# Kernel tuning notes

Measured on AMD Instinct MI355X. Metric: run time of the kernel, lower is better.

Reference implementation:

```python
import jax, jax.numpy as jnp
import numpy as np

E, S, D, A, L, H, C = 8, 6000, 128, 16, 64, 256, 64
B = 50            # no_batches hardcoded in torch forward
T = S // B        # number of outer integration steps
DT = 0.5          # solver dt; t_horizon=[0,1] -> 2 reversible-Heun substeps
NSUB = 2
SQDT = float(np.sqrt(DT))


def setup_inputs():
    ks = jax.random.split(jax.random.key(0), 24)
    w = lambda k, shp, s=0.05: (jax.random.normal(k, shp) * s).astype(jnp.float32)
    z = lambda shp: jnp.zeros(shp, jnp.float32)
    return dict(
        xs=w(ks[0], (E, S, D), 1.0),
        actions=w(ks[1], (E, S, A), 1.0),
        z0_noise=w(ks[2], (T, E, B, L), 1.0),
        dW=w(ks[3], (T, NSUB, E * B, L), 1.0),
        enc_w1=w(ks[4], (E, D, H)), enc_b1=z((E, H)),
        enc_w2=w(ks[5], (E, H, C)), enc_b2=z((E, C)),
        qz0_w=w(ks[6], (E, C, 2 * L)), qz0_b=z((E, 2 * L)),
        act_w=w(ks[7], (E, L + A + D, L)), act_b=z((E, L)),
        fw1=w(ks[8], (L, H)), fb1=z((H,)),
        fw2=w(ks[9], (H, H)), fb2=z((H,)),
        fw3=w(ks[10], (H, L)), fb3=z((L,)),
        hw1=w(ks[11], (L, H)), hb1=z((H,)),
        hw2=w(ks[12], (H, H)), hb2=z((H,)),
        hw3=w(ks[13], (H, L)), hb3=z((L,)),
        gw1=w(ks[14], (L, H)), gb1=z((L, H)),
        gw2=w(ks[15], (L, H), 0.02), gb2=jnp.ones((L,), jnp.float32),
        pw1=w(ks[16], (E, L, H)), pb1=z((E, H)),
        pw2=w(ks[17], (E, H, H)), pb2=z((E, H)),
        pw3=w(ks[18], (E, H, D)), pb3=z((E, D)),
        pz0_mean=z((E, 1, L)), pz0_logstd=z((E, 1, L)),
    )


def reference(xs, actions, z0_noise, dW,
              enc_w1, enc_b1, enc_w2, enc_b2, qz0_w, qz0_b, act_w, act_b,
              fw1, fb1, fw2, fb2, fw3, fb3, hw1, hb1, hw2, hb2, hw3, hb3,
              gw1, gb1, gw2, gb2, pw1, pb1, pw2, pb2, pw3, pb3,
              pz0_mean, pz0_logstd):
    xs_r = xs.reshape(E, T, B, D).transpose(1, 0, 2, 3)       # [T,E,B,D]
    act_r = actions.reshape(E, T, B, A).transpose(1, 0, 2, 3)  # [T,E,B,A]

    def mlp3(y, w1, b1, w2, b2, w3, b3):
        h1 = jax.nn.sigmoid(y @ w1 + b1)
        h2 = jax.nn.sigmoid(h1 @ w2 + b2)
        return h2 @ w3 + b3

    def g_fn(y):  # per-latent-dim diagonal diffusion nets, vectorized over L
        hc = jax.nn.sigmoid(y[..., None] * gw1 + gb1)          # [N,L,H]
        return jnp.sum(hc * gw2, axis=-1) + gb2                # [N,L]

    def drift_all(zc):
        fz = mlp3(zc, fw1, fb1, fw2, fb2, fw3, fb3)
        hz = mlp3(zc, hw1, hb1, hw2, hb2, hw3, hb3)
        gz = g_fn(zc)
        u = (fz - hz) / gz
        return fz, gz, 0.5 * jnp.sum(u * u, axis=-1)           # logqp drift

    def sde_solve(zini, dWs):  # reversible Heun, Stratonovich, logqp-augmented
        zc = zh = zini
        lc = lh = jnp.zeros(zini.shape[0], zini.dtype)
        fz, gz, lf = drift_all(zc)
        for k in range(NSUB):
            dWk = dWs[k] * SQDT
            zh_n = 2.0 * zc - zh + fz * DT + gz * dWk
            lh_n = 2.0 * lc - lh + lf * DT
            fz1, gz1, lf1 = drift_all(zh_n)
            zc = zc + 0.5 * (fz + fz1) * DT + 0.5 * (gz + gz1) * dWk
            lc = lc + 0.5 * (lf + lf1) * DT
            zh, lh, fz, gz, lf = zh_n, lh_n, fz1, gz1, lf1
        return zc, lc

    def step(z_prev, inp):
        i, x_i, a_i, n_i, dW_i = inp
        c1 = jax.nn.sigmoid(jnp.einsum('ebd,edh->ebh', x_i, enc_w1) + enc_b1[:, None])
        ctx = jnp.einsum('ebh,ehc->ebc', c1, enc_w2) + enc_b2[:, None]
        q = jnp.einsum('ebc,eck->ebk', ctx, qz0_w) + qz0_b[:, None]
        qm, ql = q[..., :L], q[..., L:]
        z0 = qm + jnp.exp(ql) * n_i
        z_in = jnp.where(i == 0, z0, z_prev)
        lat = jnp.concatenate([z_in, a_i, x_i], axis=-1)
        z_enc = jnp.einsum('ebf,efl->ebl', lat, act_w) + act_b[:, None]
        zf, lr = sde_solve(z_enc.reshape(E * B, L), dW_i)
        z_new = zf.reshape(E, B, L)
        p1 = jax.nn.sigmoid(jnp.einsum('ebl,elh->ebh', z_new, pw1) + pb1[:, None])
        p2 = jax.nn.sigmoid(jnp.einsum('ebh,ehk->ebk', p1, pw2) + pb2[:, None])
        xm = jnp.einsum('ebh,ehd->ebd', p2, pw3) + pb3[:, None]
        # KL(q(z0) || p(z0)) elementwise, p has mean pz0_mean, logstd pz0_logstd
        kl = (pz0_logstd - ql
              + (jnp.exp(2.0 * ql) + (qm - pz0_mean) ** 2) / (2.0 * jnp.exp(2.0 * pz0_logstd))
              - 0.5)
        logqp0 = kl.sum(-1).mean(-1)  # [E]
        return z_new, (xm, lr.reshape(E, B), logqp0)

    z_init = jnp.zeros((E, B, L), xs.dtype)
    _, (xm_all, lr_all, lq0_all) = jax.lax.scan(
        step, z_init, (jnp.arange(T), xs_r, act_r, z0_noise, dW))
    predicted_xs = xm_all.transpose(1, 0, 2, 3).reshape(E, T * B, D)
    logqp_path = lr_all.mean(-1).sum(0) + lq0_all.sum(0)  # [E]
    return logqp_path, predicted_xs
```

## Files before the change

### kernel.cpp

```cpp
#include <hip/hip_runtime.h>
#include <math.h>

#define E 8
#define S 6000
#define D 128
#define A 16
#define L 64
#define H 256
#define C 64
#define B 50
#define T 120
#define NSUB 2
#define FLAT 208
#define RTOT 400
#define RPB 10
#define NBLK (RTOT / RPB)
#define BGRP 10
#define NBG 5

#define DT 0.5f
#define SQDT 0.70710678118654752440f

#define GNT 4096
#define GYMIN (-128.0f)
#define GDY 0.0625f
#define GINVDY 16.0f

typedef __attribute__((ext_vector_type(8))) short bf16x8;
typedef __attribute__((ext_vector_type(4))) float f32x4;

#define MFMA16(a, b, c) __builtin_amdgcn_mfma_f32_16x16x32_bf16(a, b, c, 0, 0, 0)

__device__ __forceinline__ float sigf(float x) { return 1.0f / (1.0f + __expf(-x)); }

__device__ __forceinline__ unsigned short f2bf(float x) {
    union { float f; unsigned u; } v; v.f = x;
    unsigned r = (v.u + 0x7FFFu + ((v.u >> 16) & 1u)) >> 16;
    return (unsigned short)r;
}

__device__ __forceinline__ void bar_lgkm() {
    asm volatile("s_waitcnt lgkmcnt(0)" ::: "memory");
    __builtin_amdgcn_s_barrier();
    __builtin_amdgcn_sched_barrier(0);
}

__global__ void gtab_kernel(const float* __restrict__ gw1, const float* __restrict__ gb1,
                            const float* __restrict__ gw2, const float* __restrict__ gb2,
                            float* __restrict__ tab) {
    int idx = blockIdx.x * blockDim.x + threadIdx.x;
    if (idx >= L * GNT) return;
    int l = idx / GNT, i = idx % GNT;
    float y = GYMIN + (float)i * GDY;
    const float* w1 = gw1 + l * H;
    const float* b1 = gb1 + l * H;
    const float* w2 = gw2 + l * H;
    float acc = gb2[l];
    #pragma unroll 4
    for (int h = 0; h < H; ++h) acc += w2[h] * sigf(y * w1[h] + b1[h]);
    tab[idx] = acc;
}

__global__ void packB_kernel(const float* __restrict__ src, unsigned short* __restrict__ dst,
                             int K, int N) {
    int idx = blockIdx.x * 256 + threadIdx.x;
    if (idx >= K * N) return;
    int j = idx & 7;
    int lane = (idx >> 3) & 63;
    int t2 = idx >> 9;
    int KC = K >> 5;
    int kc = t2 % KC, n = t2 / KC;
    int k = (kc << 5) + ((lane >> 4) << 3) + j;
    int c = (n << 4) + (lane & 15);
    dst[idx] = f2bf(src[k * N + c]);
}

__global__ void packAW_kernel(const float* __restrict__ aw, unsigned short* __restrict__ dst) {
    int idx = blockIdx.x * 256 + threadIdx.x;
    if (idx >= E * L * L) return;
    int e = idx >> 12;
    int rem = idx & 4095;
    int j = rem & 7;
    int lane = (rem >> 3) & 63;
    int t2 = rem >> 9;
    int kc = t2 & 1, n = t2 >> 1;
    int k = (kc << 5) + ((lane >> 4) << 3) + j;
    int c = (n << 4) + (lane & 15);
    dst[idx] = f2bf(aw[((size_t)e * FLAT + k) * L + c]);
}

__global__ __launch_bounds__(256) void enc_kernel(const float* __restrict__ xs, const float* __restrict__ z0n,
                           const float* __restrict__ ew1, const float* __restrict__ eb1,
                           const float* __restrict__ ew2, const float* __restrict__ eb2,
                           const float* __restrict__ qw,  const float* __restrict__ qb,
                           const float* __restrict__ pm,  const float* __restrict__ pl,
                           float* __restrict__ z0buf, float* __restrict__ logqp0p) {
    int bid = blockIdx.x;
    int bg = bid % NBG; int te = bid / NBG; int e = te % E; int t = te / E;
    int tid = threadIdx.x;
    __shared__ float xsh[BGRP][D];
    __shared__ float c1s[BGRP][H];
    __shared__ float part[4][C][BGRP];
    __shared__ float ctxs[BGRP][C];
    __shared__ float qs[BGRP][2 * L];

    for (int i = tid; i < BGRP * D; i += 256) {
        int j = i / D, d = i % D;
        xsh[j][d] = xs[((size_t)e * S + (size_t)t * B + bg * BGRP + j) * D + d];
    }
    __syncthreads();
    {
        float bias = eb1[e * H + tid];
        float acc[BGRP];
        #pragma unroll
        for (int j = 0; j < BGRP; ++j) acc[j] = bias;
        const float* w = ew1 + (size_t)e * D * H + tid;
        #pragma unroll 4
        for (int d = 0; d < D; ++d) {
            float wv = w[(size_t)d * H];
            #pragma unroll
            for (int j = 0; j < BGRP; ++j) acc[j] += xsh[j][d] * wv;
        }
        #pragma unroll
        for (int j = 0; j < BGRP; ++j) c1s[j][tid] = sigf(acc[j]);
    }
    __syncthreads();
    {
        int c = tid & 63, kq = tid >> 6;
        float acc[BGRP];
        #pragma unroll
        for (int j = 0; j < BGRP; ++j) acc[j] = 0.f;
        const float* w = ew2 + (size_t)e * H * C + c;
        #pragma unroll 4
        for (int h = kq * 64; h < kq * 64 + 64; ++h) {
            float wv = w[(size_t)h * C];
            #pragma unroll
            for (int j = 0; j < BGRP; ++j) acc[j] += c1s[j][h] * wv;
        }
        #pragma unroll
        for (int j = 0; j < BGRP; ++j) part[kq][c][j] = acc[j];
    }
    __syncthreads();
    if (tid < C) {
        float bias = eb2[e * C + tid];
        #pragma unroll
        for (int j = 0; j < BGRP; ++j)
            ctxs[j][tid] = part[0][tid][j] + part[1][tid][j] + part[2][tid][j] + part[3][tid][j] + bias;
    }
    __syncthreads();
    if (tid < 2 * L) {
        float bias = qb[e * 2 * L + tid];
        float acc[BGRP];
        #pragma unroll
        for (int j = 0; j < BGRP; ++j) acc[j] = bias;
        const float* w = qw + (size_t)e * C * 2 * L + tid;
        #pragma unroll 4
        for (int c = 0; c < C; ++c) {
            float wv = w[(size_t)c * 2 * L];
            #pragma unroll
            for (int j = 0; j < BGRP; ++j) acc[j] += ctxs[j][c] * wv;
        }
        #pragma unroll
        for (int j = 0; j < BGRP; ++j) qs[j][tid] = acc[j];
    }
    __syncthreads();
    if (tid < L) {
        int l = tid;
        float kacc = 0.f;
        float m = pm[e * L + l], ls = pl[e * L + l];
        float inv2e = 1.0f / (2.0f * __expf(2.0f * ls));
        #pragma unroll
        for (int j = 0; j < BGRP; ++j) {
            float qm = qs[j][l], ql = qs[j][L + l];
            if (t == 0) {
                int b = bg * BGRP + j;
                float n = z0n[((size_t)e * B + b) * L + l];
                z0buf[((size_t)e * B + b) * L + l] = qm + __expf(ql) * n;
            }
            float dq = qm - m;
            kacc += ls - ql + (__expf(2.f * ql) + dq * dq) * inv2e - 0.5f;
        }
        #pragma unroll
        for (int off = 32; off; off >>= 1) kacc += __shfl_xor(kacc, off);
        if (l == 0) logqp0p[bid] = kacc / (float)B;
    }
}

__global__ __launch_bounds__(64) void ax_kernel(const float* __restrict__ xs, const float* __restrict__ actions,
                          const float* __restrict__ aw, const float* __restrict__ ab,
                          float* __restrict__ ax) {
    int bid = blockIdx.x;
    int bg = bid % NBG; int te = bid / NBG; int e = te % E; int t = te / E;
    int tid = threadIdx.x;
    __shared__ float xrow[BGRP][D];
    __shared__ float arow[BGRP][A];
    for (int i = tid; i < BGRP * D; i += 64) {
        int j = i / D, d = i % D;
        xrow[j][d] = xs[((size_t)e * S + (size_t)t * B + bg * BGRP + j) * D + d];
    }
    for (int i = tid; i < BGRP * A; i += 64) {
        int j = i / A, a = i % A;
        arow[j][a] = actions[((size_t)e * S + (size_t)t * B + bg * BGRP + j) * A + a];
    }
    __syncthreads();
    int l = tid;
    float acc[BGRP];
    float bias = ab[e * L + l];
    #pragma unroll
    for (int j = 0; j < BGRP; ++j) acc[j] = bias;
    const float* awp = aw + ((size_t)e * FLAT + L) * L + l;
    #pragma unroll 4
    for (int a = 0; a < A; ++a) {
        float wv = awp[(size_t)a * L];
        #pragma unroll
        for (int j = 0; j < BGRP; ++j) acc[j] += arow[j][a] * wv;
    }
    const float* xwp = aw + ((size_t)e * FLAT + L + A) * L + l;
    #pragma unroll 4
    for (int d = 0; d < D; ++d) {
        float wv = xwp[(size_t)d * L];
        #pragma unroll
        for (int j = 0; j < BGRP; ++j) acc[j] += xrow[j][d] * wv;
    }
    size_t rbase = (size_t)t * RTOT + e * B + bg * BGRP;
    #pragma unroll
    for (int j = 0; j < BGRP; ++j) ax[(rbase + j) * L + l] = acc[j];
}

__global__ __launch_bounds__(1024, 4) void seq_kernel(
    const unsigned short* __restrict__ pkAW, const float* __restrict__ dW,
    const float* __restrict__ z0buf, const float* __restrict__ axbuf,
    const unsigned short* __restrict__ pk1, const unsigned short* __restrict__ pk2,
    const unsigned short* __restrict__ pk3,
    const float* __restrict__ fb1, const float* __restrict__ hb1,
    const float* __restrict__ fb2, const float* __restrict__ hb2,
    const float* __restrict__ fb3, const float* __restrict__ hb3,
    const float* __restrict__ gtab, float* __restrict__ z_all, float* __restrict__ rowlr)
{
    __shared__ __align__(16) bf16x8 w1L[4096];
    __shared__ __align__(16) unsigned short ybfA[1024];
    __shared__ __align__(16) unsigned short ybfZ[1024];
    __shared__ __align__(16) unsigned short o1[2][4096];
    __shared__ __align__(16) unsigned short o2[2][4096];
    __shared__ float fh2[2][2][16][64];
    __shared__ float zcS[16][64];

    int tid = threadIdx.x;
    int wv = tid >> 6;
    int lane = tid & 63;
    int rA = lane & 15, kg = lane >> 4;
    int sw = (rA & 7) << 3;
    int r_base = blockIdx.x * RPB;
    int e = blockIdx.x / 5;

    for (int i = tid; i < 4096; i += 1024) w1L[i] = ((const bf16x8*)pk1)[i];

    int net = wv >> 3;
    int na = (wv & 7) << 1;
    int cnet = wv >> 3, crem = wv & 7, n0c = crem >> 1, khc = crem & 1;
    int nZ = wv & 3;
    int lZ = (nZ << 4) + rA;

    bf16x8 W0r0 = {}, W0r1 = {}, W2r[16], W3r[4];
    if (wv < 4) {
        const bf16x8* p0 = (const bf16x8*)pkAW + (e << 9);
        W0r0 = p0[(nZ * 2 + 0) * 64 + lane];
        W0r1 = p0[(nZ * 2 + 1) * 64 + lane];
    }
    {
        const bf16x8* p2 = (const bf16x8*)pk2 + net * 8192;
        #pragma unroll
        for (int i2 = 0; i2 < 2; ++i2)
            #pragma unroll
            for (int kc = 0; kc < 8; ++kc)
                W2r[i2 * 8 + kc] = p2[((na + i2) * 8 + kc) * 64 + lane];
        const bf16x8* p3 = (const bf16x8*)pk3 + cnet * 2048;
        #pragma unroll
        for (int kc = 0; kc < 4; ++kc)
            W3r[kc] = p3[(n0c * 8 + khc * 4 + kc) * 64 + lane];
    }
    float biasA0, biasA1, biasB0, biasB1, biasC;
    {
        const float* b1 = net ? hb1 : fb1;
        const float* b2 = net ? hb2 : fb2;
        const float* b3 = cnet ? hb3 : fb3;
        biasA0 = b1[((na + 0) << 4) + rA];
        biasA1 = b1[((na + 1) << 4) + rA];
        biasB0 = b2[((na + 0) << 4) + rA];
        biasB1 = b2[((na + 1) << 4) + rA];
        biasC = khc ? 0.f : b3[(n0c << 4) + rA];
    }

    int orow = tid >> 6, ol = tid & 63;
    bool owner = (tid < RPB * L);
    float zc_r = 0.f, zh_r = 0.f, fz_r = 0.f, gz_r = 1.f;
    float dwA_r = 0.f, dwB_r = 0.f;
    float gt0 = 1.f, gt1 = 1.f, gfr = 0.f;
    float scal = 0.f;

    {
        int r = tid >> 6;
        float v = (tid < RPB * L) ? z0buf[(size_t)r_base * L + tid] : 0.f;
        ybfZ[tid ^ ((r & 7) << 3)] = f2bf(v);
    }
    __syncthreads();

    auto gprep = [&](float v) {
        float x = (v - GYMIN) * GINVDY;
        x = fminf(fmaxf(x, 0.0f), (float)(GNT - 2) + 0.999f);
        int ii = (int)x;
        gfr = x - (float)ii;
        const float* tl = gtab + ((size_t)ol << 12);
        gt0 = tl[ii];
        gt1 = tl[ii + 1];
    };

    for (int t = 0; t < T; ++t) {
        if (wv < 4) {
            float axv[4];
            #pragma unroll
            for (int rr = 0; rr < 4; ++rr) {
                int r = (kg << 2) + rr;
                axv[rr] = (r < RPB) ? axbuf[((size_t)t * RTOT + r_base + r) * L + lZ] : 0.f;
            }
            bf16x8 Z0 = *(const bf16x8*)&ybfZ[((rA << 6) + (kg << 3)) ^ sw];
            bf16x8 Z1 = *(const bf16x8*)&ybfZ[((rA << 6) + 32 + (kg << 3)) ^ sw];
            f32x4 acc = (f32x4){0.f, 0.f, 0.f, 0.f};
            acc = MFMA16(Z0, W0r0, acc);
            acc = MFMA16(Z1, W0r1, acc);
            #pragma unroll
            for (int rr = 0; rr < 4; ++rr) {
                int r = (kg << 2) + rr;
                float v = acc[rr] + axv[rr];
                zcS[r][lZ] = v;
                ybfA[((r << 6) + lZ) ^ ((r & 7) << 3)] = f2bf(v);
            }
        }
        bar_lgkm();

        #pragma unroll
        for (int d = 0; d < 3; ++d) {
            if (d == 0 && owner) {
                zc_r = zcS[orow][ol];
                zh_r = zc_r;
                gprep(zc_r);
                dwA_r = dW[((size_t)(2 * t) * RTOT + r_base + orow) * L + ol] * SQDT;
                dwB_r = dW[((size_t)(2 * t + 1) * RTOT + r_base + orow) * L + ol] * SQDT;
            }
            {
                bf16x8 A0 = *(const bf16x8*)&ybfA[((rA << 6) + (kg << 3)) ^ sw];
                bf16x8 A1 = *(const bf16x8*)&ybfA[((rA << 6) + 32 + (kg << 3)) ^ sw];
                f32x4 acc0 = (f32x4){biasA0, biasA0, biasA0, biasA0};
                f32x4 acc1 = (f32x4){biasA1, biasA1, biasA1, biasA1};
                acc0 = MFMA16(A0, w1L[net * 2048 + ((na + 0) * 2 + 0) * 64 + lane], acc0);
                acc0 = MFMA16(A1, w1L[net * 2048 + ((na + 0) * 2 + 1) * 64 + lane], acc0);
                acc1 = MFMA16(A0, w1L[net * 2048 + ((na + 1) * 2 + 0) * 64 + lane], acc1);
                acc1 = MFMA16(A1, w1L[net * 2048 + ((na + 1) * 2 + 1) * 64 + lane], acc1);
                unsigned short* o1n = o1[net];
                int c0 = ((na + 0) << 4) + rA;
                int c1 = ((na + 1) << 4) + rA;
                #pragma unroll
                for (int rr = 0; rr < 4; ++rr) {
                    int r = (kg << 2) + rr;
                    int rx = (r & 7) << 3;
                    o1n[((r << 8) + c0) ^ rx] = f2bf(sigf(acc0[rr]));
                    o1n[((r << 8) + c1) ^ rx] = f2bf(sigf(acc1[rr]));
                }
            }
            bar_lgkm();
            {
                const unsigned short* o1n = o1[net];
                f32x4 acc0 = (f32x4){biasB0, biasB0, biasB0, biasB0};
                f32x4 acc1 = (f32x4){biasB1, biasB1, biasB1, biasB1};
                #pragma unroll
                for (int kc = 0; kc < 8; ++kc) {
                    bf16x8 Ak = *(const bf16x8*)&o1n[((rA << 8) + (kc << 5) + (kg << 3)) ^ sw];
                    acc0 = MFMA16(Ak, W2r[kc], acc0);
                    acc1 = MFMA16(Ak, W2r[8 + kc], acc1);
                }
                unsigned short* o2n = o2[net];
                int c0 = ((na + 0) << 4) + rA;
                int c1 = ((na + 1) << 4) + rA;
                #pragma unroll
                for (int rr = 0; rr < 4; ++rr) {
                    int r = (kg << 2) + rr;
                    int rx = (r & 7) << 3;
                    o2n[((r << 8) + c0) ^ rx] = f2bf(sigf(acc0[rr]));
                    o2n[((r << 8) + c1) ^ rx] = f2bf(sigf(acc1[rr]));
                }
            }
            bar_lgkm();
            {
                const unsigned short* o2n = o2[cnet];
                f32x4 acc = (f32x4){biasC, biasC, biasC, biasC};
                #pragma unroll
                for (int kc = 0; kc < 4; ++kc) {
                    bf16x8 Ak = *(const bf16x8*)&o2n[((rA << 8) + (((khc << 2) + kc) << 5) + (kg << 3)) ^ sw];
                    acc = MFMA16(Ak, W3r[kc], acc);
                }
                int c = (n0c << 4) + rA;
                #pragma unroll
                for (int rr = 0; rr < 4; ++rr)
                    fh2[cnet][khc][(kg << 2) + rr][c] = acc[rr];
            }
            bar_lgkm();
            if (owner) {
                float fv = fh2[0][0][orow][ol] + fh2[0][1][orow][ol];
                float hv = fh2[1][0][orow][ol] + fh2[1][1][orow][ol];
                float gv = gt0 * (1.0f - gfr) + gt1 * gfr;
                float uu = (fv - hv) / gv;
                float us = uu * uu;
                if (d == 0) {
                    scal += us;
                    fz_r = fv; gz_r = gv;
                    float y1 = zc_r + fv * DT + gv * dwA_r;
                    zh_r = y1;
                    ybfA[tid ^ ((orow & 7) << 3)] = f2bf(y1);
                    gprep(y1);
                } else if (d == 1) {
                    zc_r += 0.5f * (fz_r + fv) * DT + 0.5f * (gz_r + gv) * dwA_r;
                    scal += 2.0f * us;
                    float y2 = 2.f * zc_r - zh_r + fv * DT + gv * dwB_r;
                    fz_r = fv; gz_r = gv;
                    ybfA[tid ^ ((orow & 7) << 3)] = f2bf(y2);
                    gprep(y2);
                } else {
                    zc_r += 0.5f * (fz_r + fv) * DT + 0.5f * (gz_r + gv) * dwB_r;
                    scal += us;
                    z_all[((size_t)t * RTOT + r_base) * L + tid] = zc_r;
                    ybfZ[tid ^ ((orow & 7) << 3)] = f2bf(zc_r);
                }
            }
            bar_lgkm();
        }
    }
    if (owner) {
        float s = scal;
        #pragma unroll
        for (int off = 32; off; off >>= 1) s += __shfl_xor(s, off);
        if (ol == 0) rowlr[r_base + orow] = 0.25f * DT * s;
    }
}

__global__ __launch_bounds__(256) void proj_kernel(const float* __restrict__ z_all,
                            const float* __restrict__ pw1, const float* __restrict__ pb1,
                            const float* __restrict__ pw2, const float* __restrict__ pb2,
                            const float* __restrict__ pw3, const float* __restrict__ pb3,
                            float* __restrict__ out) {
    int bid = blockIdx.x;
    int bg = bid % NBG; int te = bid / NBG; int e = te % E; int t = te / E;
    int tid = threadIdx.x;
    __shared__ float zs[BGRP][L];
    __shared__ float p1s[BGRP][H];
    __shared__ float p2s[BGRP][H];
    __shared__ float part3[D][BGRP];
    size_t rbase = (size_t)t * RTOT + e * B + bg * BGRP;
    for (int i = tid; i < BGRP * L; i += 256) {
        int j = i >> 6, ll = i & 63;
        zs[j][ll] = z_all[(rbase + j) * L + ll];
    }
    __syncthreads();
    {
        float bias = pb1[e * H + tid];
        float acc[BGRP];
        #pragma unroll
        for (int j = 0; j < BGRP; ++j) acc[j] = bias;
        const float* w = pw1 + (size_t)e * L * H + tid;
        #pragma unroll 4
        for (int k = 0; k < L; ++k) {
            float wv = w[(size_t)k * H];
            #pragma unroll
            for (int j = 0; j < BGRP; ++j) acc[j] += zs[j][k] * wv;
        }
        #pragma unroll
        for (int j = 0; j < BGRP; ++j) p1s[j][tid] = sigf(acc[j]);
    }
    __syncthreads();
    {
        float bias = pb2[e * H + tid];
        float acc[BGRP];
        #pragma unroll
        for (int j = 0; j < BGRP; ++j) acc[j] = bias;
        const float* w = pw2 + (size_t)e * H * H + tid;
        #pragma unroll 4
        for (int k = 0; k < H; ++k) {
            float wv = w[(size_t)k * H];
            #pragma unroll
            for (int j = 0; j < BGRP; ++j) acc[j] += p1s[j][k] * wv;
        }
        #pragma unroll
        for (int j = 0; j < BGRP; ++j) p2s[j][tid] = sigf(acc[j]);
    }
    __syncthreads();
    float acc3[BGRP];
    {
        int dd = tid & 127, kh = tid >> 7;
        #pragma unroll
        for (int j = 0; j < BGRP; ++j) acc3[j] = 0.f;
        const float* w = pw3 + (size_t)e * H * D + dd;
        #pragma unroll 4
        for (int k = kh * 128; k < kh * 128 + 128; ++k) {
            float wv = w[(size_t)k * D];
            #pragma unroll
            for (int j = 0; j < BGRP; ++j) acc3[j] += p2s[j][k] * wv;
        }
        if (kh == 1) {
            #pragma unroll
            for (int j = 0; j < BGRP; ++j) part3[dd][j] = acc3[j];
        }
    }
    __syncthreads();
    if (tid < D) {
        float bias = pb3[e * D + tid];
        #pragma unroll
        for (int j = 0; j < BGRP; ++j) {
            out[8 + ((size_t)e * S + (size_t)t * B + bg * BGRP + j) * D + tid]
                = acc3[j] + part3[tid][j] + bias;
        }
    }
}

__global__ void fin_kernel(const float* __restrict__ logqp0p, const float* __restrict__ rowlr,
                           float* __restrict__ out) {
    int e = threadIdx.x;
    if (e < E) {
        float acc = 0.f;
        for (int t = 0; t < T; ++t)
            for (int bg = 0; bg < NBG; ++bg)
                acc += logqp0p[(t * E + e) * NBG + bg];
        float s = 0.f;
        for (int b = 0; b < B; ++b) s += rowlr[e * B + b];
        out[e] = acc + s / (float)B;
    }
}

extern "C" void kernel_launch(void* const* d_in, const int* in_sizes, int n_in,
                              void* d_out, int out_size, void* d_ws, size_t ws_size,
                              hipStream_t stream) {
    const float* xs      = (const float*)d_in[0];
    const float* actions = (const float*)d_in[1];
    const float* z0n     = (const float*)d_in[2];
    const float* dWp     = (const float*)d_in[3];
    const float* ew1     = (const float*)d_in[4];
    const float* eb1     = (const float*)d_in[5];
    const float* ew2     = (const float*)d_in[6];
    const float* eb2     = (const float*)d_in[7];
    const float* qw      = (const float*)d_in[8];
    const float* qb      = (const float*)d_in[9];
    const float* aw      = (const float*)d_in[10];
    const float* ab      = (const float*)d_in[11];
    const float* fw1     = (const float*)d_in[12];
    const float* fb1     = (const float*)d_in[13];
    const float* fw2     = (const float*)d_in[14];
    const float* fb2     = (const float*)d_in[15];
    const float* fw3     = (const float*)d_in[16];
    const float* fb3     = (const float*)d_in[17];
    const float* hw1     = (const float*)d_in[18];
    const float* hb1     = (const float*)d_in[19];
    const float* hw2     = (const float*)d_in[20];
    const float* hb2     = (const float*)d_in[21];
    const float* hw3     = (const float*)d_in[22];
    const float* hb3     = (const float*)d_in[23];
    const float* gw1     = (const float*)d_in[24];
    const float* gb1     = (const float*)d_in[25];
    const float* gw2     = (const float*)d_in[26];
    const float* gb2     = (const float*)d_in[27];
    const float* pw1     = (const float*)d_in[28];
    const float* pb1     = (const float*)d_in[29];
    const float* pw2     = (const float*)d_in[30];
    const float* pb2     = (const float*)d_in[31];
    const float* pw3     = (const float*)d_in[32];
    const float* pb3     = (const float*)d_in[33];
    const float* pm      = (const float*)d_in[34];
    const float* pl      = (const float*)d_in[35];

    float* ws      = (float*)d_ws;
    float* z0buf   = ws;
    float* axbuf   = z0buf + 25600;
    float* z_all   = axbuf + 3072000;
    float* logqp0p = z_all + 3072000;
    float* rowlr   = logqp0p + 4800;
    float* gtab    = rowlr + 400;
    unsigned short* pku = (unsigned short*)(gtab + 262144);
    unsigned short* pk1 = pku;
    unsigned short* pk2 = pk1 + 32768;
    unsigned short* pk3 = pk2 + 131072;
    unsigned short* pkAW = pk3 + 32768;
    float* out     = (float*)d_out;

    packB_kernel<<<64,  256, 0, stream>>>(fw1, pk1,          64, 256);
    packB_kernel<<<64,  256, 0, stream>>>(hw1, pk1 + 16384,  64, 256);
    packB_kernel<<<256, 256, 0, stream>>>(fw2, pk2,          256, 256);
    packB_kernel<<<256, 256, 0, stream>>>(hw2, pk2 + 65536,  256, 256);
    packB_kernel<<<64,  256, 0, stream>>>(fw3, pk3,          256, 64);
    packB_kernel<<<64,  256, 0, stream>>>(hw3, pk3 + 16384,  256, 64);
    packAW_kernel<<<128, 256, 0, stream>>>(aw, pkAW);
    gtab_kernel<<<1024, 256, 0, stream>>>(gw1, gb1, gw2, gb2, gtab);
    enc_kernel<<<T * E * NBG, 256, 0, stream>>>(xs, z0n, ew1, eb1, ew2, eb2, qw, qb, pm, pl, z0buf, logqp0p);
    ax_kernel<<<T * E * NBG, 64, 0, stream>>>(xs, actions, aw, ab, axbuf);
    seq_kernel<<<NBLK, 1024, 0, stream>>>(pkAW, dWp, z0buf, axbuf,
                                          pk1, pk2, pk3,
                                          fb1, hb1, fb2, hb2, fb3, hb3,
                                          gtab, z_all, rowlr);
    proj_kernel<<<T * E * NBG, 256, 0, stream>>>(z_all, pw1, pb1, pw2, pb2, pw3, pb3, out);
    fin_kernel<<<1, 64, 0, stream>>>(logqp0p, rowlr, out);
}
```

Before: 3.107 ms.

## Hold layer-1 weights in registers, use fast rcp sigmoid and simpler bf16 rounding

Layer-1 MFMA weight fragments now live in per-wave registers instead of a shared-memory copy, and the launch bound drops to one block per CU so more registers are available. The sigmoid uses the hardware reciprocal, the in-loop bf16 conversion uses plain round-half-up instead of round-to-nearest-even, the sched_barrier after each barrier is removed, and the MFMA sections are wrapped in s_setprio. The aim is to cut LDS traffic and ALU work on the latency-bound sequential solver, at the cost of slightly different rounding and higher register pressure.

After: 3.396 ms. 9.3% more time.

```diff
diff --git a/kernel.cpp b/kernel.cpp
--- a/kernel.cpp
+++ b/kernel.cpp
@@ -31,18 +31,18 @@
 
 #define MFMA16(a, b, c) __builtin_amdgcn_mfma_f32_16x16x32_bf16(a, b, c, 0, 0, 0)
 
-__device__ __forceinline__ float sigf(float x) { return 1.0f / (1.0f + __expf(-x)); }
+__device__ __forceinline__ float sigf(float x) {
+    return __builtin_amdgcn_rcpf(1.0f + __expf(-x));
+}
 
 __device__ __forceinline__ unsigned short f2bf(float x) {
     union { float f; unsigned u; } v; v.f = x;
-    unsigned r = (v.u + 0x7FFFu + ((v.u >> 16) & 1u)) >> 16;
-    return (unsigned short)r;
+    return (unsigned short)((v.u + 0x8000u) >> 16);
 }
 
 __device__ __forceinline__ void bar_lgkm() {
     asm volatile("s_waitcnt lgkmcnt(0)" ::: "memory");
     __builtin_amdgcn_s_barrier();
-    __builtin_amdgcn_sched_barrier(0);
 }
 
 __global__ void gtab_kernel(const float* __restrict__ gw1, const float* __restrict__ gb1,
@@ -57,7 +57,7 @@
     const float* w2 = gw2 + l * H;
     float acc = gb2[l];
     #pragma unroll 4
-    for (int h = 0; h < H; ++h) acc += w2[h] * sigf(y * w1[h] + b1[h]);
+    for (int h = 0; h < H; ++h) acc += w2[h] * (1.0f / (1.0f + __expf(-(y * w1[h] + b1[h]))));
     tab[idx] = acc;
 }
 
@@ -72,7 +72,8 @@
     int kc = t2 % KC, n = t2 / KC;
     int k = (kc << 5) + ((lane >> 4) << 3) + j;
     int c = (n << 4) + (lane & 15);
-    dst[idx] = f2bf(src[k * N + c]);
+    union { float f; unsigned u; } v; v.f = src[k * N + c];
+    dst[idx] = (unsigned short)((v.u + 0x7FFFu + ((v.u >> 16) & 1u)) >> 16);
 }
 
 __global__ void packAW_kernel(const float* __restrict__ aw, unsigned short* __restrict__ dst) {
@@ -86,7 +87,8 @@
     int kc = t2 & 1, n = t2 >> 1;
     int k = (kc << 5) + ((lane >> 4) << 3) + j;
     int c = (n << 4) + (lane & 15);
-    dst[idx] = f2bf(aw[((size_t)e * FLAT + k) * L + c]);
+    union { float f; unsigned u; } v; v.f = aw[((size_t)e * FLAT + k) * L + c];
+    dst[idx] = (unsigned short)((v.u + 0x7FFFu + ((v.u >> 16) & 1u)) >> 16);
 }
 
 __global__ __launch_bounds__(256) void enc_kernel(const float* __restrict__ xs, const float* __restrict__ z0n,
@@ -227,7 +229,7 @@
     for (int j = 0; j < BGRP; ++j) ax[(rbase + j) * L + l] = acc[j];
 }
 
-__global__ __launch_bounds__(1024, 4) void seq_kernel(
+__global__ __launch_bounds__(1024, 1) void seq_kernel(
     const unsigned short* __restrict__ pkAW, const float* __restrict__ dW,
     const float* __restrict__ z0buf, const float* __restrict__ axbuf,
     const unsigned short* __restrict__ pk1, const unsigned short* __restrict__ pk2,
@@ -237,7 +239,6 @@
     const float* __restrict__ fb3, const float* __restrict__ hb3,
     const float* __restrict__ gtab, float* __restrict__ z_all, float* __restrict__ rowlr)
 {
-    __shared__ __align__(16) bf16x8 w1L[4096];
     __shared__ __align__(16) unsigned short ybfA[1024];
     __shared__ __align__(16) unsigned short ybfZ[1024];
     __shared__ __align__(16) unsigned short o1[2][4096];
@@ -253,21 +254,23 @@
     int r_base = blockIdx.x * RPB;
     int e = blockIdx.x / 5;
 
-    for (int i = tid; i < 4096; i += 1024) w1L[i] = ((const bf16x8*)pk1)[i];
-
     int net = wv >> 3;
     int na = (wv & 7) << 1;
     int cnet = wv >> 3, crem = wv & 7, n0c = crem >> 1, khc = crem & 1;
     int nZ = wv & 3;
     int lZ = (nZ << 4) + rA;
 
-    bf16x8 W0r0 = {}, W0r1 = {}, W2r[16], W3r[4];
+    bf16x8 W0r0 = {}, W0r1 = {}, W1r[4], W2r[16], W3r[4];
     if (wv < 4) {
         const bf16x8* p0 = (const bf16x8*)pkAW + (e << 9);
         W0r0 = p0[(nZ * 2 + 0) * 64 + lane];
         W0r1 = p0[(nZ * 2 + 1) * 64 + lane];
     }
     {
+        const bf16x8* p1 = (const bf16x8*)pk1 + net * 2048;
+        #pragma unroll
+        for (int f = 0; f < 4; ++f)
+            W1r[f] = p1[((na + (f >> 1)) * 2 + (f & 1)) * 64 + lane];
         const bf16x8* p2 = (const bf16x8*)pk2 + net * 8192;
         #pragma unroll
         for (int i2 = 0; i2 < 2; ++i2)
@@ -352,10 +355,12 @@
                 bf16x8 A1 = *(const bf16x8*)&ybfA[((rA << 6) + 32 + (kg << 3)) ^ sw];
                 f32x4 acc0 = (f32x4){biasA0, biasA0, biasA0, biasA0};
                 f32x4 acc1 = (f32x4){biasA1, biasA1, biasA1, biasA1};
-                acc0 = MFMA16(A0, w1L[net * 2048 + ((na + 0) * 2 + 0) * 64 + lane], acc0);
-                acc0 = MFMA16(A1, w1L[net * 2048 + ((na + 0) * 2 + 1) * 64 + lane], acc0);
-                acc1 = MFMA16(A0, w1L[net * 2048 + ((na + 1) * 2 + 0) * 64 + lane], acc1);
-                acc1 = MFMA16(A1, w1L[net * 2048 + ((na + 1) * 2 + 1) * 64 + lane], acc1);
+                __builtin_amdgcn_s_setprio(1);
+                acc0 = MFMA16(A0, W1r[0], acc0);
+                acc0 = MFMA16(A1, W1r[1], acc0);
+                acc1 = MFMA16(A0, W1r[2], acc1);
+                acc1 = MFMA16(A1, W1r[3], acc1);
+                __builtin_amdgcn_s_setprio(0);
                 unsigned short* o1n = o1[net];
                 int c0 = ((na + 0) << 4) + rA;
                 int c1 = ((na + 1) << 4) + rA;
@@ -372,12 +377,14 @@
                 const unsigned short* o1n = o1[net];
                 f32x4 acc0 = (f32x4){biasB0, biasB0, biasB0, biasB0};
                 f32x4 acc1 = (f32x4){biasB1, biasB1, biasB1, biasB1};
+                __builtin_amdgcn_s_setprio(1);
                 #pragma unroll
                 for (int kc = 0; kc < 8; ++kc) {
                     bf16x8 Ak = *(const bf16x8*)&o1n[((rA << 8) + (kc << 5) + (kg << 3)) ^ sw];
                     acc0 = MFMA16(Ak, W2r[kc], acc0);
                     acc1 = MFMA16(Ak, W2r[8 + kc], acc1);
                 }
+                __builtin_amdgcn_s_setprio(0);
                 unsigned short* o2n = o2[net];
                 int c0 = ((na + 0) << 4) + rA;
                 int c1 = ((na + 1) << 4) + rA;
@@ -393,11 +400,13 @@
             {
                 const unsigned short* o2n = o2[cnet];
                 f32x4 acc = (f32x4){biasC, biasC, biasC, biasC};
+                __builtin_amdgcn_s_setprio(1);
                 #pragma unroll
                 for (int kc = 0; kc < 4; ++kc) {
                     bf16x8 Ak = *(const bf16x8*)&o2n[((rA << 8) + (((khc << 2) + kc) << 5) + (kg << 3)) ^ sw];
                     acc = MFMA16(Ak, W3r[kc], acc);
                 }
+                __builtin_amdgcn_s_setprio(0);
                 int c = (n0c << 4) + rA;
                 #pragma unroll
                 for (int rr = 0; rr < 4; ++rr)
```
